# Optimization experiments

Measured on AMD Instinct MI355X. Metric: run time of the kernel, lower is better.

Reference implementation:

```python
import jax, jax.numpy as jnp
import numpy as np

N, D, F, H, L = 500000, 2, 128, 128, 8
OMEGA_0 = 30.0


def setup_inputs() -> dict:
    key = jax.random.key(0)
    ks = jax.random.split(key, 13)
    two_pi = 2.0 * np.pi
    w = 0.05  # weight init scale
    return {
        "S": jax.random.uniform(ks[0], (N, 1), jnp.float32),
        "t": jax.random.uniform(ks[1], (N, 1), jnp.float32),
        "B": jax.random.normal(ks[2], (D, F), jnp.float32) * two_pi,
        "in_w": jax.random.normal(ks[3], (2 * F, H), jnp.float32) * w,
        "in_b": jax.random.normal(ks[4], (H,), jnp.float32) * w,
        "blk_w1": jax.random.normal(ks[5], (L, H, H), jnp.float32) * w,
        "blk_b1": jax.random.normal(ks[6], (L, H), jnp.float32) * w,
        "blk_w2": jax.random.normal(ks[7], (L, H, H), jnp.float32) * w,
        "blk_b2": jax.random.normal(ks[8], (L, H), jnp.float32) * w,
        "skip_w": jax.random.normal(ks[9], ((L + 1) // 2, 2 * F, H), jnp.float32) * w,
        "skip_b": jax.random.normal(ks[10], ((L + 1) // 2, H), jnp.float32) * w,
        "out_w": jax.random.normal(ks[11], (H, 1), jnp.float32) * w,
        "out_b": jax.random.normal(ks[12], (1,), jnp.float32) * w,
    }


def reference(S, t, B, in_w, in_b, blk_w1, blk_b1, blk_w2, blk_b2,
              skip_w, skip_b, out_w, out_b):
    # Fourier feature mapping: [N,2] -> [N,2F]
    inputs = jnp.concatenate([S, t], axis=1)
    proj = inputs @ B                       # [N, F]
    ff = jnp.concatenate([jnp.sin(proj), jnp.cos(proj)], axis=-1)  # [N, 2F]
    # SIREN input layer
    x = jnp.sin(OMEGA_0 * (ff @ in_w + in_b))  # [N, H]
    n_blocks = blk_w1.shape[0]
    for i in range(n_blocks):  # small fixed layer loop
        h = jnp.tanh(x @ blk_w1[i] + blk_b1[i]) @ blk_w2[i] + blk_b2[i]
        x = x + h  # residual
        if i % 2 == 0:  # periodic skip from Fourier features
            x = x + ff @ skip_w[i // 2] + skip_b[i // 2]
    return x @ out_w + out_b  # [N, 1]
```

## Files before the change

kernel.cpp:

```cpp
#include <hip/hip_runtime.h>
#include <cstdint>
#include <cstddef>

#define NPTS 500000

using f16   = _Float16;
using f16x8 = __attribute__((ext_vector_type(8))) _Float16;
using f32x4 = __attribute__((ext_vector_type(4))) float;
using f32x16= __attribute__((ext_vector_type(16))) float;

#define WS_INW   0u
#define WS_SKIP  65536u
#define WS_W1    327680u
#define WS_W2    589824u
#define WS_BIAS  851968u
#define WS_BC    863232u
#define WS_OB    864256u
#define WS_TOTAL 864272u

__device__ __host__ __forceinline__ int phi(int m) {
  return (m & ~12) | ((m & 4) << 1) | ((m & 8) >> 1);
}
__device__ __forceinline__ uint32_t swz(uint32_t off, uint32_t row, uint32_t mask) {
  return off ^ ((row & mask) << 4);
}

extern "C" __global__ void pinn_prep(const float* __restrict__ in_w,
                                     const float* __restrict__ w1,
                                     const float* __restrict__ w2,
                                     const float* __restrict__ skw,
                                     const float* __restrict__ inb,
                                     const float* __restrict__ b1,
                                     const float* __restrict__ b2,
                                     const float* __restrict__ skb,
                                     const float* __restrict__ ow,
                                     const float* __restrict__ ob,
                                     const float* __restrict__ Bg,
                                     char* __restrict__ ws) {
  int idx = (int)blockIdx.x * 256 + (int)threadIdx.x;
  if (idx < 32768) {
    int m = idx >> 8, c = idx & 255;
    int k = ((c >> 4) & 1) * 128 + (c >> 5) * 16 + (c & 15);
    uint32_t off = swz((uint32_t)(m * 512 + c * 2), (uint32_t)m, 31u);
    *(f16*)(ws + WS_INW + off) = (f16)in_w[k * 128 + phi(m)];
  } else if (idx < 163840) {
    int r = idx - 32768; int j = r >> 15; r &= 32767;
    int m = r >> 8, c = r & 255;
    int k = ((c >> 4) & 1) * 128 + (c >> 5) * 16 + (c & 15);
    uint32_t off = swz((uint32_t)(m * 512 + c * 2), (uint32_t)m, 31u);
    *(f16*)(ws + WS_SKIP + (uint32_t)j * 65536u + off) = (f16)skw[(j * 256 + k) * 128 + phi(m)];
  } else if (idx < 425984) {
    int r = idx - 163840;
    const int isw2 = (r >= 131072);
    int rr = r & 131071;
    int i = rr >> 14; int q = rr & 16383;
    int m = q >> 7, k = q & 127;
    uint32_t off = swz((uint32_t)(m * 256 + k * 2), (uint32_t)m, 15u);
    uint32_t base = (isw2 ? WS_W2 : WS_W1) + (uint32_t)i * 32768u;
    const float* src = isw2 ? w2 : w1;
    *(f16*)(ws + base + off) = (f16)src[(i * 128 + k) * 128 + phi(m)];
  } else if (idx < 428800) {
    int r = idx - 425984;
    int M = r >> 7, pos = r & 127;
    int pp = phi(pos);
    float v;
    if (M == 0)        v = inb[pp];
    else if (M <= 16)  { int t = M - 1; int i = t >> 1; v = (t & 1) ? b2[i * 128 + pp] : b1[i * 128 + pp]; }
    else if (M <= 20)  v = skb[(M - 17) * 128 + pp];
    else               v = ow[pp];
    *(float*)(ws + WS_BIAS + (uint32_t)r * 4u) = v;
  } else if (idx < 429056) {
    int r = idx - 428800;
    int slot = r >> 4, e2 = r & 15;
    int kq = slot >> 1, hb = slot & 1;
    int row = e2 >> 3, e = e2 & 7;
    int j = kq * 16 + hb * 8 + e;
    *(float*)(ws + WS_BC + (uint32_t)r * 4u) = Bg[row * 128 + j] * 0.15915494309189535f;
  } else if (idx == 429056) {
    *(float*)(ws + WS_OB) = ob[0];
    *(float*)(ws + WS_OB + 4) = 0.f; *(float*)(ws + WS_OB + 8) = 0.f; *(float*)(ws + WS_OB + 12) = 0.f;
  }
}

__device__ __forceinline__ float ftanh(float x) {
  float e = __builtin_amdgcn_exp2f(x * 2.8853901817f);
  return 1.0f - 2.0f * __builtin_amdgcn_rcpf(e + 1.0f);
}
__device__ __forceinline__ float fsin_rev(float rev) {
  return __builtin_amdgcn_sinf(__builtin_amdgcn_fractf(rev));
}

__device__ __forceinline__ void gll16(const char* g, char* l) {
  __builtin_amdgcn_global_load_lds((const __attribute__((address_space(1))) void*)g,
                                   (__attribute__((address_space(3))) void*)l, 16, 0, 0);
}
__device__ __forceinline__ void stage64(const char* g, char* l, int wv, int ln64) {
  const char* gs = g + wv * 8192 + ln64 * 16;
  char* ls = l + wv * 8192;
  #pragma unroll
  for (int it = 0; it < 8; ++it) gll16(gs + it * 1024, ls + it * 1024);
}
__device__ __forceinline__ void stage32(const char* g, char* l, int wv, int ln64) {
  const char* gs = g + wv * 4096 + ln64 * 16;
  char* ls = l + wv * 4096;
  #pragma unroll
  for (int it = 0; it < 4; ++it) gll16(gs + it * 1024, ls + it * 1024);
}

#define MFMA_(a,b,c) __builtin_amdgcn_mfma_f32_32x32x16_f16(a,b,c,0,0,0)

#define LD256(BASE, MT, KB) (*(const f16x8*)((BASE) + \
  swz(((uint32_t)(MT)*32u + lnr)*256u + (uint32_t)(KB)*32u + hi16, lnr, 15u)))
#define LD512(BASE, MT, KB) (*(const f16x8*)((BASE) + \
  swz(((uint32_t)(MT)*32u + lnr)*512u + (uint32_t)(KB)*32u + hi16, lnr, 31u)))

#define BINIT(acc, Mi, MT) { const float* _bp = biasL + ((Mi)*128 + (MT)*32 + hi4); \
  f32x4 _q0 = *(const f32x4*)_bp;        f32x4 _q1 = *(const f32x4*)(_bp+8); \
  f32x4 _q2 = *(const f32x4*)(_bp+16);   f32x4 _q3 = *(const f32x4*)(_bp+24); \
  acc[0]=_q0[0]; acc[1]=_q0[1]; acc[2]=_q0[2]; acc[3]=_q0[3]; \
  acc[4]=_q1[0]; acc[5]=_q1[1]; acc[6]=_q1[2]; acc[7]=_q1[3]; \
  acc[8]=_q2[0]; acc[9]=_q2[1]; acc[10]=_q2[2]; acc[11]=_q2[3]; \
  acc[12]=_q3[0]; acc[13]=_q3[1]; acc[14]=_q3[2]; acc[15]=_q3[3]; }

#define UNPADD(acc, F0, F1) { \
  acc[0]+=(float)F0[0]; acc[1]+=(float)F0[1]; acc[2]+=(float)F0[2]; acc[3]+=(float)F0[3]; \
  acc[4]+=(float)F0[4]; acc[5]+=(float)F0[5]; acc[6]+=(float)F0[6]; acc[7]+=(float)F0[7]; \
  acc[8]+=(float)F1[0]; acc[9]+=(float)F1[1]; acc[10]+=(float)F1[2]; acc[11]+=(float)F1[3]; \
  acc[12]+=(float)F1[4]; acc[13]+=(float)F1[5]; acc[14]+=(float)F1[6]; acc[15]+=(float)F1[7]; }

#define FPACK(F0, F1, acc) { f16x8 _g0, _g1; \
  _g0[0]=(f16)acc[0]; _g0[1]=(f16)acc[1]; _g0[2]=(f16)acc[2]; _g0[3]=(f16)acc[3]; \
  _g0[4]=(f16)acc[4]; _g0[5]=(f16)acc[5]; _g0[6]=(f16)acc[6]; _g0[7]=(f16)acc[7]; \
  _g1[0]=(f16)acc[8]; _g1[1]=(f16)acc[9]; _g1[2]=(f16)acc[10]; _g1[3]=(f16)acc[11]; \
  _g1[4]=(f16)acc[12]; _g1[5]=(f16)acc[13]; _g1[6]=(f16)acc[14]; _g1[7]=(f16)acc[15]; \
  F0=_g0; F1=_g1; }

#define TPACK(F0, F1, acc) { f16x8 _g0, _g1; \
  _g0[0]=(f16)ftanh(acc[0]); _g0[1]=(f16)ftanh(acc[1]); _g0[2]=(f16)ftanh(acc[2]); _g0[3]=(f16)ftanh(acc[3]); \
  _g0[4]=(f16)ftanh(acc[4]); _g0[5]=(f16)ftanh(acc[5]); _g0[6]=(f16)ftanh(acc[6]); _g0[7]=(f16)ftanh(acc[7]); \
  _g1[0]=(f16)ftanh(acc[8]); _g1[1]=(f16)ftanh(acc[9]); _g1[2]=(f16)ftanh(acc[10]); _g1[3]=(f16)ftanh(acc[11]); \
  _g1[4]=(f16)ftanh(acc[12]); _g1[5]=(f16)ftanh(acc[13]); _g1[6]=(f16)ftanh(acc[14]); _g1[7]=(f16)ftanh(acc[15]); \
  F0=_g0; F1=_g1; }

#define OM2PI 4.7746482927f
#define SINPACK(F0, F1, acc) { f16x8 _g0, _g1; \
  _g0[0]=(f16)fsin_rev(acc[0]*OM2PI); _g0[1]=(f16)fsin_rev(acc[1]*OM2PI); \
  _g0[2]=(f16)fsin_rev(acc[2]*OM2PI); _g0[3]=(f16)fsin_rev(acc[3]*OM2PI); \
  _g0[4]=(f16)fsin_rev(acc[4]*OM2PI); _g0[5]=(f16)fsin_rev(acc[5]*OM2PI); \
  _g0[6]=(f16)fsin_rev(acc[6]*OM2PI); _g0[7]=(f16)fsin_rev(acc[7]*OM2PI); \
  _g1[0]=(f16)fsin_rev(acc[8]*OM2PI); _g1[1]=(f16)fsin_rev(acc[9]*OM2PI); \
  _g1[2]=(f16)fsin_rev(acc[10]*OM2PI); _g1[3]=(f16)fsin_rev(acc[11]*OM2PI); \
  _g1[4]=(f16)fsin_rev(acc[12]*OM2PI); _g1[5]=(f16)fsin_rev(acc[13]*OM2PI); \
  _g1[6]=(f16)fsin_rev(acc[14]*OM2PI); _g1[7]=(f16)fsin_rev(acc[15]*OM2PI); \
  F0=_g0; F1=_g1; }

#define FFE(ei, CA, CB) { \
  float _r0 = __builtin_amdgcn_fractf(s0v*(CA) + t0v*(CB)); \
  _s0[ei]=(f16)__builtin_amdgcn_sinf(_r0); _c0[ei]=(f16)__builtin_amdgcn_cosf(_r0); \
  float _r1 = __builtin_amdgcn_fractf(s1v*(CA) + t1v*(CB)); \
  _s1[ei]=(f16)__builtin_amdgcn_sinf(_r1); _c1[ei]=(f16)__builtin_amdgcn_cosf(_r1); }
#define FF2(G, FSA, FCA, FSB, FCB) { const float* _cp = BcL + ((G)*2+hi)*16; \
  f32x4 _a0 = *(const f32x4*)_cp, _a1 = *(const f32x4*)(_cp+4); \
  f32x4 _b0 = *(const f32x4*)(_cp+8), _b1 = *(const f32x4*)(_cp+12); \
  f16x8 _s0, _c0, _s1, _c1; \
  FFE(0,_a0[0],_b0[0]) FFE(1,_a0[1],_b0[1]) FFE(2,_a0[2],_b0[2]) FFE(3,_a0[3],_b0[3]) \
  FFE(4,_a1[0],_b1[0]) FFE(5,_a1[1],_b1[1]) FFE(6,_a1[2],_b1[2]) FFE(7,_a1[3],_b1[3]) \
  FSA=_s0; FCA=_c0; FSB=_s1; FCB=_c1; }

#define FFPASS(M0_, M1_, MI_, XA0,XA1, XB0,XB1, YA0,YA1, YB0,YB1, RES, SINEPI) { \
  f32x16 a00; BINIT(a00, MI_, M0_); f32x16 a01 = a00; \
  f32x16 a10; BINIT(a10, MI_, M1_); f32x16 a11 = a10; \
  if (RES) { UNPADD(a00, XA0, XA1) UNPADD(a01, XB0, XB1) \
             UNPADD(a10, YA0, YA1) UNPADD(a11, YB0, YB1) } \
  for (int g = 0; g < 8; ++g) { \
    f16x8 fsA, fcA, fsB, fcB; \
    FF2(g, fsA, fcA, fsB, fcB) \
    { f16x8 _w = LD512(sb_, M0_, 2*g);   a00 = MFMA_(_w, fsA, a00); a01 = MFMA_(_w, fsB, a01); } \
    { f16x8 _w = LD512(sb_, M0_, 2*g+1); a00 = MFMA_(_w, fcA, a00); a01 = MFMA_(_w, fcB, a01); } \
    { f16x8 _w = LD512(sb_, M1_, 2*g);   a10 = MFMA_(_w, fsA, a10); a11 = MFMA_(_w, fsB, a11); } \
    { f16x8 _w = LD512(sb_, M1_, 2*g+1); a10 = MFMA_(_w, fcA, a10); a11 = MFMA_(_w, fcB, a11); } \
  } \
  if (SINEPI) { SINPACK(XA0, XA1, a00) SINPACK(XB0, XB1, a01) \
                SINPACK(YA0, YA1, a10) SINPACK(YB0, YB1, a11) } \
  else        { FPACK(XA0, XA1, a00) FPACK(XB0, XB1, a01) \
                FPACK(YA0, YA1, a10) FPACK(YB0, YB1, a11) } }

#define W1K(kb) { f16x8 _a = LD256(wb, MTv, kb); \
  acc0 = MFMA_(_a, xA##kb, acc0); acc1 = MFMA_(_a, xB##kb, acc1); }
#define W2K(kb) { f16x8 _a = LD256(wb2, MTv, kb); \
  acc0 = MFMA_(_a, uA##kb, acc0); acc1 = MFMA_(_a, uB##kb, acc1); }

#define W1TILE(MT, UA0_, UA1_, UB0_, UB1_) { const uint32_t MTv = (MT); \
  f32x16 acc0; BINIT(acc0, Mw1, MT); f32x16 acc1 = acc0; \
  W1K(0) W1K(1) W1K(2) W1K(3) W1K(4) W1K(5) W1K(6) W1K(7) \
  TPACK(UA0_, UA1_, acc0); TPACK(UB0_, UB1_, acc1); }

#define W2TILE(MT, XA0_, XA1_, XB0_, XB1_) { const uint32_t MTv = (MT); \
  f32x16 acc0; BINIT(acc0, Mw2, MT); f32x16 acc1 = acc0; \
  UNPADD(acc0, XA0_, XA1_); UNPADD(acc1, XB0_, XB1_); \
  W2K(0) W2K(1) W2K(2) W2K(3) W2K(4) W2K(5) W2K(6) W2K(7) \
  FPACK(XA0_, XA1_, acc0); FPACK(XB0_, XB1_, acc1); }

#define OWDOT(P, F0, F1, bp) P += (float)F0[0]*bp[0] + (float)F0[1]*bp[1] + (float)F0[2]*bp[2] + (float)F0[3]*bp[3] \
  + (float)F0[4]*bp[8]  + (float)F0[5]*bp[9]  + (float)F0[6]*bp[10] + (float)F0[7]*bp[11] \
  + (float)F1[0]*bp[16] + (float)F1[1]*bp[17] + (float)F1[2]*bp[18] + (float)F1[3]*bp[19] \
  + (float)F1[4]*bp[24] + (float)F1[5]*bp[25] + (float)F1[6]*bp[26] + (float)F1[7]*bp[27];

extern "C" __global__ void
__attribute__((amdgpu_flat_work_group_size(512, 512), amdgpu_waves_per_eu(2, 2)))
pinn_main(const float* __restrict__ Sg, const float* __restrict__ Tg,
          const char* __restrict__ ws, float* __restrict__ outg)
{
  extern __shared__ char smem[];
  const float* biasL = (const float*)(smem + 131072);
  const float* BcL   = biasL + 2816;

  const int tid  = (int)threadIdx.x;
  const int lane = tid & 63;
  const int wave = tid >> 6;
  const int hi   = lane >> 5;
  const uint32_t lnr = (uint32_t)(lane & 31);
  const uint32_t hi16 = (uint32_t)hi * 16u;
  const int hi4  = hi * 4;
  const int blk0 = (int)blockIdx.x * 512;

  const int pb = blk0 + wave * 64 + (int)lnr;
  const int q0 = pb      < NPTS ? pb      : NPTS - 1;
  const int q1 = pb + 32 < NPTS ? pb + 32 : NPTS - 1;
  const float s0v = Sg[q0], t0v = Tg[q0];
  const float s1v = Sg[q1], t1v = Tg[q1];

  #pragma unroll 1
  for (int o = tid * 16; o < 12304; o += 8192)
    *(f32x4*)(smem + 131072 + o) = *(const f32x4*)(ws + WS_BIAS + o);
  stage64(ws + WS_INW, smem, wave, lane);
  __syncthreads();

  f16x8 xA0,xA1,xA2,xA3,xA4,xA5,xA6,xA7, xB0,xB1,xB2,xB3,xB4,xB5,xB6,xB7;
  f16x8 uA0,uA1,uA2,uA3,uA4,uA5,uA6,uA7, uB0,uB1,uB2,uB3,uB4,uB5,uB6,uB7;

  stage32(ws + WS_W1, smem + 65536, wave, lane);
  stage32(ws + WS_W2, smem + 65536 + 32768, wave, lane);

  {
    const char* sb_ = smem;
    FFPASS(0, 1, 0, xA0,xA1, xB0,xB1, xA2,xA3, xB2,xB3, 0, 1)
    FFPASS(2, 3, 0, xA4,xA5, xB4,xB5, xA6,xA7, xB6,xB7, 0, 1)
  }
  __syncthreads();

  #pragma unroll 1
  for (int i = 0; i < 8; ++i) {
    const int wbix = ((i >> 1) & 1) ^ 1;
    const char* wb  = smem + wbix * 65536;
    const char* wb2 = wb + 32768;
    const int Mw1 = 1 + 2 * i, Mw2 = 2 + 2 * i;

    if ((i & 1) == 0) {
      const int j = i >> 1;
      stage64(ws + WS_SKIP + (uint32_t)j * 65536u, smem + (j & 1) * 65536, wave, lane);
    } else if (i < 7) {
      const int bix = (((i + 1) >> 1) & 1) ^ 1;
      stage32(ws + WS_W1 + (uint32_t)(i + 1) * 32768u, smem + bix * 65536, wave, lane);
      stage32(ws + WS_W2 + (uint32_t)(i + 1) * 32768u, smem + bix * 65536 + 32768, wave, lane);
    }

    W1TILE(0, uA0, uA1, uB0, uB1)
    W1TILE(1, uA2, uA3, uB2, uB3)
    W1TILE(2, uA4, uA5, uB4, uB5)
    W1TILE(3, uA6, uA7, uB6, uB7)
    W2TILE(0, xA0, xA1, xB0, xB1)
    W2TILE(1, xA2, xA3, xB2, xB3)
    W2TILE(2, xA4, xA5, xB4, xB5)
    W2TILE(3, xA6, xA7, xB6, xB7)
    __syncthreads();

    if ((i & 1) == 0) {
      const int j = i >> 1;
      const int bix2 = (((i + 1) >> 1) & 1) ^ 1;
      stage32(ws + WS_W1 + (uint32_t)(i + 1) * 32768u, smem + bix2 * 65536, wave, lane);
      stage32(ws + WS_W2 + (uint32_t)(i + 1) * 32768u, smem + bix2 * 65536 + 32768, wave, lane);
      const int Msk = 17 + j;
      const char* sb_ = smem + (j & 1) * 65536;
      FFPASS(0, 1, Msk, xA0,xA1, xB0,xB1, xA2,xA3, xB2,xB3, 1, 0)
      FFPASS(2, 3, Msk, xA4,xA5, xB4,xB5, xA6,xA7, xB6,xB7, 1, 0)
      __syncthreads();
    }
  }

  float p0 = 0.0f, p1 = 0.0f;
  { const float* bp = biasL + 21 * 128 + 0 * 32 + hi4; OWDOT(p0, xA0, xA1, bp) OWDOT(p1, xB0, xB1, bp) }
  { const float* bp = biasL + 21 * 128 + 1 * 32 + hi4; OWDOT(p0, xA2, xA3, bp) OWDOT(p1, xB2, xB3, bp) }
  { const float* bp = biasL + 21 * 128 + 2 * 32 + hi4; OWDOT(p0, xA4, xA5, bp) OWDOT(p1, xB4, xB5, bp) }
  { const float* bp = biasL + 21 * 128 + 3 * 32 + hi4; OWDOT(p0, xA6, xA7, bp) OWDOT(p1, xB6, xB7, bp) }
  p0 += __shfl_xor(p0, 32);
  p1 += __shfl_xor(p1, 32);
  const float obv = biasL[3072];
  if (hi == 0) {
    if (pb < NPTS)      outg[pb]      = p0 + obv;
    if (pb + 32 < NPTS) outg[pb + 32] = p1 + obv;
  }
}

extern "C" void kernel_launch(void* const* d_in, const int* in_sizes, int n_in,
                              void* d_out, int out_size, void* d_ws, size_t ws_size,
                              hipStream_t stream) {
  (void)in_sizes; (void)n_in; (void)out_size;
  const float* S   = (const float*)d_in[0];
  const float* T   = (const float*)d_in[1];
  const float* B   = (const float*)d_in[2];
  const float* inw = (const float*)d_in[3];
  const float* inb = (const float*)d_in[4];
  const float* w1  = (const float*)d_in[5];
  const float* b1  = (const float*)d_in[6];
  const float* w2  = (const float*)d_in[7];
  const float* b2  = (const float*)d_in[8];
  const float* sw  = (const float*)d_in[9];
  const float* sb  = (const float*)d_in[10];
  const float* ow  = (const float*)d_in[11];
  const float* ob  = (const float*)d_in[12];
  char* ws   = (char*)d_ws;
  float* out = (float*)d_out;
  if (ws_size < (size_t)WS_TOTAL) return;

  pinn_prep<<<1677, 256, 0, stream>>>(inw, w1, w2, sw, inb, b1, b2, sb, ow, ob, B, ws);

  const int smem_bytes = 143376;
  hipFuncSetAttribute(reinterpret_cast<const void*>(pinn_main),
                      hipFuncAttributeMaxDynamicSharedMemorySize, smem_bytes);
  const int grid = (NPTS + 511) / 512;
  pinn_main<<<grid, 512, smem_bytes, stream>>>(S, T, ws, out);
}
```

Baseline: 577.8 us.

## Halve per-wave points and LDS footprint to raise occupancy

Each wave now processes 32 points instead of 64, which halves the register-held activation state. LDS use drops from two 64KB weight double-buffers to two 32KB slots, and skip and input weights are split into halves that are staged between passes. The goal is to fit more workgroups per CU (launch bounds 512,4) and hide latency through occupancy rather than in-block double-buffering. The cost is extra barriers, serialized staging with less prefetch overlap, and half the MFMA reuse of each loaded weight fragment.

Measured after the change: 805.4 us. 1.39x slower.

```diff
diff --git a/kernel.cpp b/kernel.cpp
--- a/kernel.cpp
+++ b/kernel.cpp
@@ -20,9 +20,6 @@
 
 __device__ __host__ __forceinline__ int phi(int m) {
   return (m & ~12) | ((m & 4) << 1) | ((m & 8) >> 1);
-}
-__device__ __forceinline__ uint32_t swz(uint32_t off, uint32_t row, uint32_t mask) {
-  return off ^ ((row & mask) << 4);
 }
 
 extern "C" __global__ void pinn_prep(const float* __restrict__ in_w,
@@ -39,26 +36,30 @@
                                      char* __restrict__ ws) {
   int idx = (int)blockIdx.x * 256 + (int)threadIdx.x;
   if (idx < 32768) {
-    int m = idx >> 8, c = idx & 255;
-    int k = ((c >> 4) & 1) * 128 + (c >> 5) * 16 + (c & 15);
-    uint32_t off = swz((uint32_t)(m * 512 + c * 2), (uint32_t)m, 31u);
-    *(f16*)(ws + WS_INW + off) = (f16)in_w[k * 128 + phi(m)];
+    int H = idx >> 14, r = idx & 16383, m = r >> 7, c = r & 127;
+    int gl = c >> 5, sc = (c >> 4) & 1, lo = c & 15;
+    int k = sc * 128 + (H * 4 + gl) * 16 + lo;
+    uint32_t off = (uint32_t)(m * 256 + c * 2) ^ (uint32_t)((m & 15) << 4);
+    *(f16*)(ws + WS_INW + (uint32_t)H * 32768u + off) = (f16)in_w[k * 128 + phi(m)];
   } else if (idx < 163840) {
-    int r = idx - 32768; int j = r >> 15; r &= 32767;
-    int m = r >> 8, c = r & 255;
-    int k = ((c >> 4) & 1) * 128 + (c >> 5) * 16 + (c & 15);
-    uint32_t off = swz((uint32_t)(m * 512 + c * 2), (uint32_t)m, 31u);
-    *(f16*)(ws + WS_SKIP + (uint32_t)j * 65536u + off) = (f16)skw[(j * 256 + k) * 128 + phi(m)];
+    int r0 = idx - 32768;
+    int j4 = r0 >> 15, rr = r0 & 32767;
+    int H = rr >> 14, r = rr & 16383, m = r >> 7, c = r & 127;
+    int gl = c >> 5, sc = (c >> 4) & 1, lo = c & 15;
+    int k = sc * 128 + (H * 4 + gl) * 16 + lo;
+    uint32_t off = (uint32_t)(m * 256 + c * 2) ^ (uint32_t)((m & 15) << 4);
+    *(f16*)(ws + WS_SKIP + (uint32_t)j4 * 65536u + (uint32_t)H * 32768u + off) =
+        (f16)skw[(j4 * 256 + k) * 128 + phi(m)];
+  } else if (idx < 294912) {
+    int r0 = idx - 163840;
+    int i = r0 >> 14, r = r0 & 16383, m = r >> 7, k = r & 127;
+    uint32_t off = (uint32_t)(m * 256 + k * 2) ^ (uint32_t)((m & 15) << 4);
+    *(f16*)(ws + WS_W1 + (uint32_t)i * 32768u + off) = (f16)w1[(i * 128 + k) * 128 + phi(m)];
   } else if (idx < 425984) {
-    int r = idx - 163840;
-    const int isw2 = (r >= 131072);
-    int rr = r & 131071;
-    int i = rr >> 14; int q = rr & 16383;
-    int m = q >> 7, k = q & 127;
-    uint32_t off = swz((uint32_t)(m * 256 + k * 2), (uint32_t)m, 15u);
-    uint32_t base = (isw2 ? WS_W2 : WS_W1) + (uint32_t)i * 32768u;
-    const float* src = isw2 ? w2 : w1;
-    *(f16*)(ws + base + off) = (f16)src[(i * 128 + k) * 128 + phi(m)];
+    int r0 = idx - 294912;
+    int i = r0 >> 14, r = r0 & 16383, m = r >> 7, k = r & 127;
+    uint32_t off = (uint32_t)(m * 256 + k * 2) ^ (uint32_t)((m & 15) << 4);
+    *(f16*)(ws + WS_W2 + (uint32_t)i * 32768u + off) = (f16)w2[(i * 128 + k) * 128 + phi(m)];
   } else if (idx < 428800) {
     int r = idx - 425984;
     int M = r >> 7, pos = r & 127;
@@ -94,12 +95,6 @@
   __builtin_amdgcn_global_load_lds((const __attribute__((address_space(1))) void*)g,
                                    (__attribute__((address_space(3))) void*)l, 16, 0, 0);
 }
-__device__ __forceinline__ void stage64(const char* g, char* l, int wv, int ln64) {
-  const char* gs = g + wv * 8192 + ln64 * 16;
-  char* ls = l + wv * 8192;
-  #pragma unroll
-  for (int it = 0; it < 8; ++it) gll16(gs + it * 1024, ls + it * 1024);
-}
 __device__ __forceinline__ void stage32(const char* g, char* l, int wv, int ln64) {
   const char* gs = g + wv * 4096 + ln64 * 16;
   char* ls = l + wv * 4096;
@@ -107,12 +102,10 @@
   for (int it = 0; it < 4; ++it) gll16(gs + it * 1024, ls + it * 1024);
 }
 
-#define MFMA_(a,b,c) __builtin_amdgcn_mfma_f32_32x32x16_f16(a,b,c,0,0,0)
-
-#define LD256(BASE, MT, KB) (*(const f16x8*)((BASE) + \
-  swz(((uint32_t)(MT)*32u + lnr)*256u + (uint32_t)(KB)*32u + hi16, lnr, 15u)))
-#define LD512(BASE, MT, KB) (*(const f16x8*)((BASE) + \
-  swz(((uint32_t)(MT)*32u + lnr)*512u + (uint32_t)(KB)*32u + hi16, lnr, 31u)))
+#define MFMA_(a,b,c)  __builtin_amdgcn_mfma_f32_32x32x16_f16(a,b,c,0,0,0)
+
+#define LDW(BASE, MT, KB) (*(const f16x8*)((BASE) + \
+  ((((uint32_t)(MT)*32u + lnr)*256u + (uint32_t)(KB)*32u + hi16v) ^ SW16)))
 
 #define BINIT(acc, Mi, MT) { const float* _bp = biasL + ((Mi)*128 + (MT)*32 + hi4); \
   f32x4 _q0 = *(const f32x4*)_bp;        f32x4 _q1 = *(const f32x4*)(_bp+8); \
@@ -155,151 +148,126 @@
   F0=_g0; F1=_g1; }
 
 #define FFE(ei, CA, CB) { \
-  float _r0 = __builtin_amdgcn_fractf(s0v*(CA) + t0v*(CB)); \
-  _s0[ei]=(f16)__builtin_amdgcn_sinf(_r0); _c0[ei]=(f16)__builtin_amdgcn_cosf(_r0); \
-  float _r1 = __builtin_amdgcn_fractf(s1v*(CA) + t1v*(CB)); \
-  _s1[ei]=(f16)__builtin_amdgcn_sinf(_r1); _c1[ei]=(f16)__builtin_amdgcn_cosf(_r1); }
-#define FF2(G, FSA, FCA, FSB, FCB) { const float* _cp = BcL + ((G)*2+hi)*16; \
+  float _r = __builtin_amdgcn_fractf(sv*(CA) + tv*(CB)); \
+  _s[ei] = (f16)__builtin_amdgcn_sinf(_r); _c[ei] = (f16)__builtin_amdgcn_cosf(_r); }
+#define FF2(G, FS, FC) { const float* _cp = BcL + ((G)*2 + hi)*16; \
   f32x4 _a0 = *(const f32x4*)_cp, _a1 = *(const f32x4*)(_cp+4); \
   f32x4 _b0 = *(const f32x4*)(_cp+8), _b1 = *(const f32x4*)(_cp+12); \
-  f16x8 _s0, _c0, _s1, _c1; \
+  f16x8 _s, _c; \
   FFE(0,_a0[0],_b0[0]) FFE(1,_a0[1],_b0[1]) FFE(2,_a0[2],_b0[2]) FFE(3,_a0[3],_b0[3]) \
   FFE(4,_a1[0],_b1[0]) FFE(5,_a1[1],_b1[1]) FFE(6,_a1[2],_b1[2]) FFE(7,_a1[3],_b1[3]) \
-  FSA=_s0; FCA=_c0; FSB=_s1; FCB=_c1; }
-
-#define FFPASS(M0_, M1_, MI_, XA0,XA1, XB0,XB1, YA0,YA1, YB0,YB1, RES, SINEPI) { \
-  f32x16 a00; BINIT(a00, MI_, M0_); f32x16 a01 = a00; \
-  f32x16 a10; BINIT(a10, MI_, M1_); f32x16 a11 = a10; \
-  if (RES) { UNPADD(a00, XA0, XA1) UNPADD(a01, XB0, XB1) \
-             UNPADD(a10, YA0, YA1) UNPADD(a11, YB0, YB1) } \
-  for (int g = 0; g < 8; ++g) { \
-    f16x8 fsA, fcA, fsB, fcB; \
-    FF2(g, fsA, fcA, fsB, fcB) \
-    { f16x8 _w = LD512(sb_, M0_, 2*g);   a00 = MFMA_(_w, fsA, a00); a01 = MFMA_(_w, fsB, a01); } \
-    { f16x8 _w = LD512(sb_, M0_, 2*g+1); a00 = MFMA_(_w, fcA, a00); a01 = MFMA_(_w, fcB, a01); } \
-    { f16x8 _w = LD512(sb_, M1_, 2*g);   a10 = MFMA_(_w, fsA, a10); a11 = MFMA_(_w, fsB, a11); } \
-    { f16x8 _w = LD512(sb_, M1_, 2*g+1); a10 = MFMA_(_w, fcA, a10); a11 = MFMA_(_w, fcB, a11); } \
-  } \
-  if (SINEPI) { SINPACK(XA0, XA1, a00) SINPACK(XB0, XB1, a01) \
-                SINPACK(YA0, YA1, a10) SINPACK(YB0, YB1, a11) } \
-  else        { FPACK(XA0, XA1, a00) FPACK(XB0, XB1, a01) \
-                FPACK(YA0, YA1, a10) FPACK(YB0, YB1, a11) } }
-
-#define W1K(kb) { f16x8 _a = LD256(wb, MTv, kb); \
-  acc0 = MFMA_(_a, xA##kb, acc0); acc1 = MFMA_(_a, xB##kb, acc1); }
-#define W2K(kb) { f16x8 _a = LD256(wb2, MTv, kb); \
-  acc0 = MFMA_(_a, uA##kb, acc0); acc1 = MFMA_(_a, uB##kb, acc1); }
-
-#define W1TILE(MT, UA0_, UA1_, UB0_, UB1_) { const uint32_t MTv = (MT); \
-  f32x16 acc0; BINIT(acc0, Mw1, MT); f32x16 acc1 = acc0; \
+  FS = _s; FC = _c; }
+
+#define FFG(G, SLOT) { f16x8 _fs,_fc; FF2(G,_fs,_fc) \
+  { f16x8 _w=LDW(SLOT,0,((G)&3)*2);   a0=MFMA_(_w,_fs,a0); } \
+  { f16x8 _w=LDW(SLOT,0,((G)&3)*2+1); a0=MFMA_(_w,_fc,a0); } \
+  { f16x8 _w=LDW(SLOT,1,((G)&3)*2);   a1=MFMA_(_w,_fs,a1); } \
+  { f16x8 _w=LDW(SLOT,1,((G)&3)*2+1); a1=MFMA_(_w,_fc,a1); } \
+  { f16x8 _w=LDW(SLOT,2,((G)&3)*2);   a2=MFMA_(_w,_fs,a2); } \
+  { f16x8 _w=LDW(SLOT,2,((G)&3)*2+1); a2=MFMA_(_w,_fc,a2); } \
+  { f16x8 _w=LDW(SLOT,3,((G)&3)*2);   a3=MFMA_(_w,_fs,a3); } \
+  { f16x8 _w=LDW(SLOT,3,((G)&3)*2+1); a3=MFMA_(_w,_fc,a3); } }
+
+#define W1K(kb) { f16x8 _a = LDW(sA_, MTv, kb); acc = MFMA_(_a, x##kb, acc); }
+#define W1TILE(MT, U0, U1) { const uint32_t MTv = (MT); \
+  f32x16 acc; BINIT(acc, Mw1, MT) \
   W1K(0) W1K(1) W1K(2) W1K(3) W1K(4) W1K(5) W1K(6) W1K(7) \
-  TPACK(UA0_, UA1_, acc0); TPACK(UB0_, UB1_, acc1); }
-
-#define W2TILE(MT, XA0_, XA1_, XB0_, XB1_) { const uint32_t MTv = (MT); \
-  f32x16 acc0; BINIT(acc0, Mw2, MT); f32x16 acc1 = acc0; \
-  UNPADD(acc0, XA0_, XA1_); UNPADD(acc1, XB0_, XB1_); \
+  TPACK(U0, U1, acc) }
+
+#define W2K(kb) { f16x8 _a = LDW(sB_, MTv, kb); acc = MFMA_(_a, u##kb, acc); }
+#define W2TILE(MT, X0, X1) { const uint32_t MTv = (MT); \
+  f32x16 acc; BINIT(acc, Mw2, MT) \
   W2K(0) W2K(1) W2K(2) W2K(3) W2K(4) W2K(5) W2K(6) W2K(7) \
-  FPACK(XA0_, XA1_, acc0); FPACK(XB0_, XB1_, acc1); }
+  f16x8 _t0,_t1; FPACK(_t0,_t1,acc) X0 = X0 + _t0; X1 = X1 + _t1; }
 
 #define OWDOT(P, F0, F1, bp) P += (float)F0[0]*bp[0] + (float)F0[1]*bp[1] + (float)F0[2]*bp[2] + (float)F0[3]*bp[3] \
   + (float)F0[4]*bp[8]  + (float)F0[5]*bp[9]  + (float)F0[6]*bp[10] + (float)F0[7]*bp[11] \
   + (float)F1[0]*bp[16] + (float)F1[1]*bp[17] + (float)F1[2]*bp[18] + (float)F1[3]*bp[19] \
   + (float)F1[4]*bp[24] + (float)F1[5]*bp[25] + (float)F1[6]*bp[26] + (float)F1[7]*bp[27];
 
-extern "C" __global__ void
-__attribute__((amdgpu_flat_work_group_size(512, 512), amdgpu_waves_per_eu(2, 2)))
+extern "C" __global__ void __launch_bounds__(512, 4)
 pinn_main(const float* __restrict__ Sg, const float* __restrict__ Tg,
           const char* __restrict__ ws, float* __restrict__ outg)
 {
   extern __shared__ char smem[];
-  const float* biasL = (const float*)(smem + 131072);
+  char* sAw = smem;          const char* sA_ = sAw;
+  char* sBw = smem + 32768;  const char* sB_ = sBw;
+  const float* biasL = (const float*)(smem + 65536);
   const float* BcL   = biasL + 2816;
 
   const int tid  = (int)threadIdx.x;
   const int lane = tid & 63;
   const int wave = tid >> 6;
   const int hi   = lane >> 5;
-  const uint32_t lnr = (uint32_t)(lane & 31);
-  const uint32_t hi16 = (uint32_t)hi * 16u;
+  const uint32_t lnr   = (uint32_t)(lane & 31);
+  const uint32_t hi16v = (uint32_t)hi * 16u;
+  const uint32_t SW16  = (lnr & 15u) << 4;
   const int hi4  = hi * 4;
-  const int blk0 = (int)blockIdx.x * 512;
-
-  const int pb = blk0 + wave * 64 + (int)lnr;
-  const int q0 = pb      < NPTS ? pb      : NPTS - 1;
-  const int q1 = pb + 32 < NPTS ? pb + 32 : NPTS - 1;
-  const float s0v = Sg[q0], t0v = Tg[q0];
-  const float s1v = Sg[q1], t1v = Tg[q1];
+
+  const int pt = (int)blockIdx.x * 256 + wave * 32 + (int)lnr;
+  const int q  = pt < NPTS ? pt : NPTS - 1;
+  const float sv = Sg[q], tv = Tg[q];
 
   #pragma unroll 1
   for (int o = tid * 16; o < 12304; o += 8192)
-    *(f32x4*)(smem + 131072 + o) = *(const f32x4*)(ws + WS_BIAS + o);
-  stage64(ws + WS_INW, smem, wave, lane);
+    *(f32x4*)(smem + 65536 + o) = *(const f32x4*)(ws + WS_BIAS + o);
+  stage32(ws + WS_INW,          sAw, wave, lane);
+  stage32(ws + WS_INW + 32768u, sBw, wave, lane);
   __syncthreads();
 
-  f16x8 xA0,xA1,xA2,xA3,xA4,xA5,xA6,xA7, xB0,xB1,xB2,xB3,xB4,xB5,xB6,xB7;
-  f16x8 uA0,uA1,uA2,uA3,uA4,uA5,uA6,uA7, uB0,uB1,uB2,uB3,uB4,uB5,uB6,uB7;
-
-  stage32(ws + WS_W1, smem + 65536, wave, lane);
-  stage32(ws + WS_W2, smem + 65536 + 32768, wave, lane);
+  f16x8 x0,x1,x2,x3,x4,x5,x6,x7;
+  f16x8 u0,u1,u2,u3,u4,u5,u6,u7;
 
   {
-    const char* sb_ = smem;
-    FFPASS(0, 1, 0, xA0,xA1, xB0,xB1, xA2,xA3, xB2,xB3, 0, 1)
-    FFPASS(2, 3, 0, xA4,xA5, xB4,xB5, xA6,xA7, xB6,xB7, 0, 1)
+    f32x16 a0,a1,a2,a3;
+    BINIT(a0,0,0) BINIT(a1,0,1) BINIT(a2,0,2) BINIT(a3,0,3)
+    FFG(0, sA_) FFG(1, sA_) FFG(2, sA_) FFG(3, sA_)
+    __syncthreads();
+    stage32(ws + WS_W1, sAw, wave, lane);
+    FFG(4, sB_) FFG(5, sB_) FFG(6, sB_) FFG(7, sB_)
+    __syncthreads();
+    stage32(ws + WS_W2, sBw, wave, lane);
+    SINPACK(x0,x1,a0) SINPACK(x2,x3,a1) SINPACK(x4,x5,a2) SINPACK(x6,x7,a3)
   }
-  __syncthreads();
 
   #pragma unroll 1
   for (int i = 0; i < 8; ++i) {
-    const int wbix = ((i >> 1) & 1) ^ 1;
-    const char* wb  = smem + wbix * 65536;
-    const char* wb2 = wb + 32768;
     const int Mw1 = 1 + 2 * i, Mw2 = 2 + 2 * i;
 
+    __syncthreads();
+    W1TILE(0, u0,u1) W1TILE(1, u2,u3) W1TILE(2, u4,u5) W1TILE(3, u6,u7)
+    __syncthreads();
+    if ((i & 1) == 0) stage32(ws + WS_SKIP + (uint32_t)(i >> 1) * 65536u, sAw, wave, lane);
+    else if (i < 7)   stage32(ws + WS_W1 + (uint32_t)(i + 1) * 32768u, sAw, wave, lane);
+
+    W2TILE(0, x0,x1) W2TILE(1, x2,x3) W2TILE(2, x4,x5) W2TILE(3, x6,x7)
+    __syncthreads();
+    if ((i & 1) == 0) stage32(ws + WS_SKIP + (uint32_t)(i >> 1) * 65536u + 32768u, sBw, wave, lane);
+    else if (i < 7)   stage32(ws + WS_W2 + (uint32_t)(i + 1) * 32768u, sBw, wave, lane);
+
     if ((i & 1) == 0) {
-      const int j = i >> 1;
-      stage64(ws + WS_SKIP + (uint32_t)j * 65536u, smem + (j & 1) * 65536, wave, lane);
-    } else if (i < 7) {
-      const int bix = (((i + 1) >> 1) & 1) ^ 1;
-      stage32(ws + WS_W1 + (uint32_t)(i + 1) * 32768u, smem + bix * 65536, wave, lane);
-      stage32(ws + WS_W2 + (uint32_t)(i + 1) * 32768u, smem + bix * 65536 + 32768, wave, lane);
-    }
-
-    W1TILE(0, uA0, uA1, uB0, uB1)
-    W1TILE(1, uA2, uA3, uB2, uB3)
-    W1TILE(2, uA4, uA5, uB4, uB5)
-    W1TILE(3, uA6, uA7, uB6, uB7)
-    W2TILE(0, xA0, xA1, xB0, xB1)
-    W2TILE(1, xA2, xA3, xB2, xB3)
-    W2TILE(2, xA4, xA5, xB4, xB5)
-    W2TILE(3, xA6, xA7, xB6, xB7)
-    __syncthreads();
-
-    if ((i & 1) == 0) {
-      const int j = i >> 1;
-      const int bix2 = (((i + 1) >> 1) & 1) ^ 1;
-      stage32(ws + WS_W1 + (uint32_t)(i + 1) * 32768u, smem + bix2 * 65536, wave, lane);
-      stage32(ws + WS_W2 + (uint32_t)(i + 1) * 32768u, smem + bix2 * 65536 + 32768, wave, lane);
-      const int Msk = 17 + j;
-      const char* sb_ = smem + (j & 1) * 65536;
-      FFPASS(0, 1, Msk, xA0,xA1, xB0,xB1, xA2,xA3, xB2,xB3, 1, 0)
-      FFPASS(2, 3, Msk, xA4,xA5, xB4,xB5, xA6,xA7, xB6,xB7, 1, 0)
+      const int Msk = 17 + (i >> 1);
       __syncthreads();
+      f32x16 a0,a1,a2,a3;
+      BINIT(a0,Msk,0) BINIT(a1,Msk,1) BINIT(a2,Msk,2) BINIT(a3,Msk,3)
+      UNPADD(a0, x0,x1) UNPADD(a1, x2,x3) UNPADD(a2, x4,x5) UNPADD(a3, x6,x7)
+      FFG(0, sA_) FFG(1, sA_) FFG(2, sA_) FFG(3, sA_)
+      __syncthreads();
+      stage32(ws + WS_W1 + (uint32_t)(i + 1) * 32768u, sAw, wave, lane);
+      FFG(4, sB_) FFG(5, sB_) FFG(6, sB_) FFG(7, sB_)
+      __syncthreads();
+      stage32(ws + WS_W2 + (uint32_t)(i + 1) * 32768u, sBw, wave, lane);
+      FPACK(x0,x1,a0) FPACK(x2,x3,a1) FPACK(x4,x5,a2) FPACK(x6,x7,a3)
     }
   }
 
-  float p0 = 0.0f, p1 = 0.0f;
-  { const float* bp = biasL + 21 * 128 + 0 * 32 + hi4; OWDOT(p0, xA0, xA1, bp) OWDOT(p1, xB0, xB1, bp) }
-  { const float* bp = biasL + 21 * 128 + 1 * 32 + hi4; OWDOT(p0, xA2, xA3, bp) OWDOT(p1, xB2, xB3, bp) }
-  { const float* bp = biasL + 21 * 128 + 2 * 32 + hi4; OWDOT(p0, xA4, xA5, bp) OWDOT(p1, xB4, xB5, bp) }
-  { const float* bp = biasL + 21 * 128 + 3 * 32 + hi4; OWDOT(p0, xA6, xA7, bp) OWDOT(p1, xB6, xB7, bp) }
-  p0 += __shfl_xor(p0, 32);
-  p1 += __shfl_xor(p1, 32);
-  const float obv = biasL[3072];
-  if (hi == 0) {
-    if (pb < NPTS)      outg[pb]      = p0 + obv;
-    if (pb + 32 < NPTS) outg[pb + 32] = p1 + obv;
-  }
+  float p = 0.0f;
+  { const float* bp = biasL + 21 * 128 + 0 * 32 + hi4; OWDOT(p, x0, x1, bp) }
+  { const float* bp = biasL + 21 * 128 + 1 * 32 + hi4; OWDOT(p, x2, x3, bp) }
+  { const float* bp = biasL + 21 * 128 + 2 * 32 + hi4; OWDOT(p, x4, x5, bp) }
+  { const float* bp = biasL + 21 * 128 + 3 * 32 + hi4; OWDOT(p, x6, x7, bp) }
+  p += __shfl_xor(p, 32);
+  if (hi == 0 && pt < NPTS) outg[pt] = p + biasL[3072];
 }
 
 extern "C" void kernel_launch(void* const* d_in, const int* in_sizes, int n_in,
@@ -325,9 +293,9 @@
 
   pinn_prep<<<1677, 256, 0, stream>>>(inw, w1, w2, sw, inb, b1, b2, sb, ow, ob, B, ws);
 
-  const int smem_bytes = 143376;
+  const int smem_bytes = 77840;
   hipFuncSetAttribute(reinterpret_cast<const void*>(pinn_main),
                       hipFuncAttributeMaxDynamicSharedMemorySize, smem_bytes);
-  const int grid = (NPTS + 511) / 512;
+  const int grid = (NPTS + 255) / 256;
   pinn_main<<<grid, 512, smem_bytes, stream>>>(S, T, ws, out);
 }
```
